# Performance work log

Measured on AMD Instinct MI355X. Metric: run time of the kernel, lower is better.

## Reference

```python
import jax, jax.numpy as jnp
import numpy as np
from jax.ops import segment_sum

N_NODES = 50000
N_EDGES = 50000
N_GRAPHS = 1024


def _inv_deg(idx, num_segments):
    deg = segment_sum(jnp.ones(idx.shape[0], jnp.float32), idx, num_segments=num_segments)
    return jnp.where(deg > 0, 1.0 / deg, 0.0)


def hypergraph_conv(x, W, b, node_idx, edge_idx):
    # PyG HypergraphConv (use_attention=False, heads=1, hyperedge_weight=1):
    # out = D^{-1} H B^{-1} H^T (X W) + b
    D = _inv_deg(node_idx, N_NODES)   # inverse node degree [N]
    B = _inv_deg(edge_idx, N_EDGES)   # inverse hyperedge degree [E]
    xl = x @ W                         # [N, out]
    # node -> hyperedge aggregation
    edge_feat = B[:, None] * segment_sum(xl[node_idx], edge_idx, num_segments=N_EDGES)
    # hyperedge -> node aggregation
    out = D[:, None] * segment_sum(edge_feat[edge_idx], node_idx, num_segments=N_NODES)
    return out + b


def global_mean_pool(x, batch):
    s = segment_sum(x, batch, num_segments=N_GRAPHS)
    cnt = segment_sum(jnp.ones(x.shape[0], jnp.float32), batch, num_segments=N_GRAPHS)
    return s / jnp.maximum(cnt, 1.0)[:, None]


def setup_inputs() -> dict:
    key = jax.random.key(0)
    ks = jax.random.split(key, 16)
    F, H = 128, 256
    def lin(k, fi, fo):
        s = 1.0 / np.sqrt(fi)
        k1, k2 = jax.random.split(k)
        return (jax.random.uniform(k1, (fi, fo), jnp.float32, -s, s),
                jax.random.uniform(k2, (fo,), jnp.float32, -s, s))
    W1, b1 = lin(ks[0], F, H)
    W2, b2 = lin(ks[1], H, 2 * H)
    W3, b3 = lin(ks[2], 2 * H, H)
    Wl1, bl1 = lin(ks[3], H, H // 2)
    Wl2, bl2 = lin(ks[4], H // 2, 1)
    x = jax.random.normal(ks[5], (N_NODES, F), jnp.float32)
    hyperedge_index = jax.random.randint(ks[6], (2, 400000), 0, N_EDGES, jnp.int64)
    batch = jnp.sort(jax.random.randint(ks[7], (N_NODES,), 0, N_GRAPHS, jnp.int64))
    return {"x": x, "hyperedge_index": hyperedge_index, "batch": batch,
            "W1": W1, "b1": b1, "W2": W2, "b2": b2, "W3": W3, "b3": b3,
            "Wl1": Wl1, "bl1": bl1, "Wl2": Wl2, "bl2": bl2}


def reference(x, hyperedge_index, batch, W1, b1, W2, b2, W3, b3, Wl1, bl1, Wl2, bl2):
    node_idx, edge_idx = hyperedge_index[0], hyperedge_index[1]
    h = jax.nn.relu(hypergraph_conv(x, W1, b1, node_idx, edge_idx))
    h = jax.nn.relu(hypergraph_conv(h, W2, b2, node_idx, edge_idx))
    h = jax.nn.relu(hypergraph_conv(h, W3, b3, node_idx, edge_idx))
    g = global_mean_pool(h, batch)              # [G, H]
    g = jax.nn.relu(g @ Wl1 + bl1)
    out = g @ Wl2 + bl2                          # [G, 1]
    return out
```

## Files before the change

### kernel.cpp

```cpp
#include <hip/hip_runtime.h>
#include <hip/hip_bf16.h>

#define N_NODES  50000
#define N_EDGES  50000
#define N_INC    400000
#define N_GRAPHS 1024
#define M_PAD    50048
#define SEG_CAP  50176

typedef __bf16 bf16x8 __attribute__((ext_vector_type(8)));
typedef float  f32x4  __attribute__((ext_vector_type(4)));

__device__ __forceinline__ unsigned short f2bf(float f) {
    __hip_bfloat16 h = __float2bfloat16(f);
    return __builtin_bit_cast(unsigned short, h);
}
__device__ __forceinline__ float bflo(unsigned int u) {
    return __builtin_bit_cast(float, u << 16);
}
__device__ __forceinline__ float bfhi(unsigned int u) {
    return __builtin_bit_cast(float, u & 0xffff0000u);
}
__device__ __forceinline__ unsigned int packbf(float a, float b) {
    return (unsigned int)f2bf(a) | ((unsigned int)f2bf(b) << 16);
}
__device__ __forceinline__ void load_lds16(const unsigned short* g, unsigned short* l) {
    __builtin_amdgcn_global_load_lds((const __attribute__((address_space(1))) void*)g,
                                     (__attribute__((address_space(3))) void*)l, 16, 0, 0);
}

__global__ __launch_bounds__(256) void normhist_kernel(const int* __restrict__ hei,
                                                       const int* __restrict__ braw,
                                                       int* __restrict__ nidx, int* __restrict__ eidx,
                                                       int* __restrict__ bidx,
                                                       int* __restrict__ ndeg, int* __restrict__ edeg,
                                                       int* __restrict__ gcnt) {
    __shared__ int s32;
    int t = threadIdx.x;
    if (t == 0) s32 = 0;
    __syncthreads();
    int probe = hei[4 * t + 1] | hei[4 * t + 3];
    if (probe) s32 = 1;
    __syncthreads();
    int is32 = s32;
    int i = blockIdx.x * 256 + t;
    if (i < N_INC) {
        int n, e;
        if (is32) { n = hei[i];     e = hei[N_INC + i]; }
        else      { n = hei[2 * i]; e = hei[2 * N_INC + 2 * i]; }
        nidx[i] = n; eidx[i] = e;
        atomicAdd(&ndeg[n], 1);
        atomicAdd(&edeg[e], 1);
    }
    if (i < N_NODES) {
        int b = is32 ? braw[i] : braw[2 * i];
        bidx[i] = b;
        atomicAdd(&gcnt[b], 1);
    }
}

__global__ __launch_bounds__(256) void scan_up_f(const int* __restrict__ edeg,
                                                 const int* __restrict__ ndeg,
                                                 const int* __restrict__ gcnt,
                                                 int* __restrict__ eoff, int* __restrict__ noff,
                                                 int* __restrict__ goff,
                                                 int* __restrict__ partials) {
    __shared__ int lds[256];
    int b = blockIdx.x, t = threadIdx.x;
    const int* in; int* outp; int lb;
    if (b < 49)      { in = edeg; outp = eoff; lb = b; }
    else if (b < 98) { in = ndeg; outp = noff; lb = b - 49; }
    else             { in = gcnt; outp = goff; lb = 0; }
    int base = lb * 1024 + t * 4;
    int4 v = *(const int4*)(in + base);
    int s = v.x + v.y + v.z + v.w;
    lds[t] = s;
    __syncthreads();
    for (int off = 1; off < 256; off <<= 1) {
        int u = (t >= off) ? lds[t - off] : 0;
        __syncthreads();
        lds[t] += u;
        __syncthreads();
    }
    int excl = lds[t] - s;
    if (t == 255) partials[b] = lds[255];
    int4 o;
    o.x = excl;
    o.y = excl + v.x;
    o.z = o.y + v.y;
    o.w = o.z + v.z;
    *(int4*)(outp + base) = o;
}

__global__ __launch_bounds__(128) void scan_mid_f(int* __restrict__ partials) {
    __shared__ int lds[99];
    int t = threadIdx.x;
    if (t < 99) lds[t] = partials[t];
    __syncthreads();
    if (t < 3) {
        int lo = (t == 0) ? 0 : (t == 1 ? 49 : 98);
        int hi = (t == 0) ? 49 : (t == 1 ? 98 : 99);
        int run = 0;
        for (int i = lo; i < hi; ++i) { int x = lds[i]; lds[i] = run; run += x; }
    }
    __syncthreads();
    if (t < 99) partials[t] = lds[t];
}

__global__ __launch_bounds__(256) void scan_down_f(int* __restrict__ eoff, int* __restrict__ ecur,
                                                   int* __restrict__ noff, int* __restrict__ ncur,
                                                   int* __restrict__ goff,
                                                   const int* __restrict__ partials) {
    int b = blockIdx.x, t = threadIdx.x;
    int* outp; int* out2; int lb;
    if (b < 49)      { outp = eoff; out2 = ecur; lb = b; }
    else if (b < 98) { outp = noff; out2 = ncur; lb = b - 49; }
    else             { outp = goff; out2 = goff; lb = 0; }
    int base = lb * 1024 + t * 4;
    int p = partials[b];
    int4 v = *(const int4*)(outp + base);
    v.x += p; v.y += p; v.z += p; v.w += p;
    *(int4*)(outp + base) = v;
    *(int4*)(out2 + base) = v;
}

#define NB_CSR  1563
#define NB_CONV 6250
#define NB_W1   128
#define NB_W2   512
#define NB_W3   512
__global__ __launch_bounds__(256) void prep_kernel(const int* __restrict__ nidx,
                                                   const int* __restrict__ eidx,
                                                   int* __restrict__ ecur, int* __restrict__ ncur,
                                                   int* __restrict__ csre, int* __restrict__ csrn,
                                                   const float* __restrict__ x,
                                                   unsigned short* __restrict__ xbf,
                                                   const float* __restrict__ W1, unsigned short* __restrict__ wt1,
                                                   const float* __restrict__ W2, unsigned short* __restrict__ wt2,
                                                   const float* __restrict__ W3, unsigned short* __restrict__ wt3) {
    int b = blockIdx.x, t = threadIdx.x;
    if (b < NB_CSR) {
        int i = b * 256 + t;
        if (i < N_INC) {
            int n = nidx[i], e = eidx[i];
            int p = atomicAdd(&ecur[e], 1);
            csre[p] = n;
            int q = atomicAdd(&ncur[n], 1);
            csrn[q] = e;
        }
    } else if (b < NB_CSR + NB_CONV) {
        int i = (b - NB_CSR) * 256 + t;
        float4 v = *(const float4*)(x + 4 * (size_t)i);
        ushort4 o;
        o.x = f2bf(v.x); o.y = f2bf(v.y); o.z = f2bf(v.z); o.w = f2bf(v.w);
        *(ushort4*)(xbf + 4 * (size_t)i) = o;
    } else if (b < NB_CSR + NB_CONV + NB_W1) {
        int i = (b - NB_CSR - NB_CONV) * 256 + t;
        int k = i >> 8, n = i & 255;
        wt1[n * 128 + k] = f2bf(W1[i]);
    } else if (b < NB_CSR + NB_CONV + NB_W1 + NB_W2) {
        int i = (b - NB_CSR - NB_CONV - NB_W1) * 256 + t;
        int k = i >> 9, n = i & 511;
        wt2[n * 256 + k] = f2bf(W2[i]);
    } else {
        int i = (b - NB_CSR - NB_CONV - NB_W1 - NB_W2) * 256 + t;
        int k = i >> 8, n = i & 255;
        wt3[n * 512 + k] = f2bf(W3[i]);
    }
}

template <bool EPI>
__global__ __launch_bounds__(256) void gemm128_kernel(const unsigned short* __restrict__ A,
                                                      const unsigned short* __restrict__ Bt,
                                                      const float* __restrict__ bias,
                                                      unsigned short* __restrict__ C,
                                                      int M, int K, int N) {
    __shared__ unsigned short As[128 * 32];
    __shared__ unsigned short Bs[128 * 32];
    __shared__ unsigned short Cs[32][140];
    int tid  = threadIdx.x;
    int wave = tid >> 6, lane = tid & 63;
    int n0 = blockIdx.x * 128, m0 = blockIdx.y * 128;
    int quad = lane >> 4, fr = lane & 15;
    int wr = wave >> 1, wc = wave & 1;
    int lrow16 = lane >> 2;
    int lchunk = (lane & 3) * 8;

    const unsigned short* gsrc;
    unsigned short* ldst;
    if (wave < 2) { gsrc = A  + (size_t)(m0 + wave * 64) * K;       ldst = As + wave * 64 * 32; }
    else          { gsrc = Bt + (size_t)(n0 + (wave - 2) * 64) * K; ldst = Bs + (wave - 2) * 64 * 32; }

    f32x4 acc[4][4];
#pragma unroll
    for (int s = 0; s < 4; ++s)
#pragma unroll
        for (int c = 0; c < 4; ++c) acc[s][c] = (f32x4){0.f, 0.f, 0.f, 0.f};

    for (int k0 = 0; k0 < K; k0 += 32) {
#pragma unroll
        for (int l = 0; l < 4; ++l) {
            const unsigned short* g = gsrc + (size_t)(l * 16 + lrow16) * K + k0 + lchunk;
            load_lds16(g, ldst + l * 16 * 32);
        }
        __syncthreads();
        bf16x8 af[4], bfr[4];
#pragma unroll
        for (int s = 0; s < 4; ++s)
            af[s] = *(const bf16x8*)&As[(wr * 64 + s * 16 + fr) * 32 + quad * 8];
#pragma unroll
        for (int c = 0; c < 4; ++c)
            bfr[c] = *(const bf16x8*)&Bs[(wc * 64 + c * 16 + fr) * 32 + quad * 8];
#pragma unroll
        for (int s = 0; s < 4; ++s)
#pragma unroll
            for (int c = 0; c < 4; ++c)
                acc[s][c] = __builtin_amdgcn_mfma_f32_16x16x32_bf16(af[s], bfr[c], acc[s][c], 0, 0, 0);
        __syncthreads();
    }

    float bv[4];
#pragma unroll
    for (int c = 0; c < 4; ++c) bv[c] = EPI ? bias[n0 + wc * 64 + c * 16 + fr] : 0.f;
#pragma unroll
    for (int s = 0; s < 4; ++s) {
#pragma unroll
        for (int c = 0; c < 4; ++c)
#pragma unroll
            for (int r = 0; r < 4; ++r) {
                float v = acc[s][c][r];
                if (EPI) v = fmaxf(v + bv[c], 0.f);
                Cs[wr * 16 + quad * 4 + r][wc * 64 + c * 16 + fr] = f2bf(v);
            }
        __syncthreads();
#pragma unroll
        for (int i = 0; i < 2; ++i) {
            int rl  = i * 16 + (tid >> 4);
            int col = (tid & 15) * 8;
            int gm  = m0 + (rl >> 4) * 64 + s * 16 + (rl & 15);
            if (gm < M) {
                uint4 v = *(const uint4*)&Cs[rl][col];
                *(uint4*)&C[(size_t)gm * N + n0 + col] = v;
            }
        }
        __syncthreads();
    }
}

template <int C, bool BIAS>
__device__ __forceinline__ void seg_body(const unsigned short* __restrict__ in,
                                         const int* __restrict__ offs,
                                         const int* __restrict__ degs,
                                         const int* __restrict__ csr_src,
                                         const float* __restrict__ bias,
                                         unsigned short* __restrict__ outp,
                                         int nseg) {
    constexpr int VEC = C / 64;
    constexpr int NW  = VEC / 2;
    int w = (blockIdx.x * 256 + threadIdx.x) >> 6;
    int lane = threadIdx.x & 63;
    if (w >= nseg) return;
    int deg   = __builtin_amdgcn_readfirstlane(degs[w]);
    int start = __builtin_amdgcn_readfirstlane(offs[w]);
    float dinv = (deg > 0) ? 1.0f / (float)deg : 0.0f;
    const int* cs = csr_src + start;
    float acc[VEC];
#pragma unroll
    for (int q = 0; q < VEC; ++q) acc[q] = 0.f;
    size_t lbase = (size_t)lane * VEC;

    auto accum = [&](unsigned int* v) {
#pragma unroll
        for (int q = 0; q < NW; ++q) { acc[2 * q] += bflo(v[q]); acc[2 * q + 1] += bfhi(v[q]); }
    };
    auto loadrow = [&](int src, unsigned int* v) {
        const unsigned int* p = (const unsigned int*)(in + (size_t)src * C + lbase);
        if constexpr (NW == 4)      { uint4 t = *(const uint4*)p; v[0] = t.x; v[1] = t.y; v[2] = t.z; v[3] = t.w; }
        else if constexpr (NW == 2) { uint2 t = *(const uint2*)p; v[0] = t.x; v[1] = t.y; }
        else                        { v[0] = *p; }
    };

    int j = 0;
    for (; j + 8 <= deg; j += 8) {
        int s[8];
        unsigned int v[8][NW];
#pragma unroll
        for (int u = 0; u < 8; ++u) s[u] = __builtin_amdgcn_readfirstlane(cs[j + u]);
#pragma unroll
        for (int u = 0; u < 8; ++u) loadrow(s[u], v[u]);
#pragma unroll
        for (int u = 0; u < 8; ++u) accum(v[u]);
    }
    for (; j + 4 <= deg; j += 4) {
        int s[4];
        unsigned int v[4][NW];
#pragma unroll
        for (int u = 0; u < 4; ++u) s[u] = __builtin_amdgcn_readfirstlane(cs[j + u]);
#pragma unroll
        for (int u = 0; u < 4; ++u) loadrow(s[u], v[u]);
#pragma unroll
        for (int u = 0; u < 4; ++u) accum(v[u]);
    }
    for (; j < deg; ++j) {
        int s0 = __builtin_amdgcn_readfirstlane(cs[j]);
        unsigned int v0[NW];
        loadrow(s0, v0);
        accum(v0);
    }

    unsigned int o[NW];
#pragma unroll
    for (int q = 0; q < NW; ++q) {
        float a = acc[2 * q] * dinv;
        float b = acc[2 * q + 1] * dinv;
        if constexpr (BIAS) {
            a = fmaxf(a + bias[lbase + 2 * q], 0.f);
            b = fmaxf(b + bias[lbase + 2 * q + 1], 0.f);
        }
        o[q] = packbf(a, b);
    }
    unsigned int* po = (unsigned int*)(outp + (size_t)w * C + lbase);
    if constexpr (NW == 4)      { *(uint4*)po = make_uint4(o[0], o[1], o[2], o[3]); }
    else if constexpr (NW == 2) { *(uint2*)po = make_uint2(o[0], o[1]); }
    else                        { *po = o[0]; }
}

template <int C>
__global__ __launch_bounds__(256) void seg_edge_t(const unsigned short* __restrict__ xl,
                                                  const int* __restrict__ eoff,
                                                  const int* __restrict__ edeg,
                                                  const int* __restrict__ csr_src,
                                                  unsigned short* __restrict__ ef) {
    seg_body<C, false>(xl, eoff, edeg, csr_src, nullptr, ef, N_EDGES);
}

template <int C, bool BIAS>
__global__ __launch_bounds__(256) void seg_node_t(const unsigned short* __restrict__ ef,
                                                  const int* __restrict__ noff,
                                                  const int* __restrict__ ndeg,
                                                  const int* __restrict__ csr_src,
                                                  const float* __restrict__ bias,
                                                  unsigned short* __restrict__ hout) {
    seg_body<C, BIAS>(ef, noff, ndeg, csr_src, bias, hout, N_NODES);
}

__global__ __launch_bounds__(256) void pool_head_kernel(const unsigned short* __restrict__ h,
                                                        const int* __restrict__ goff,
                                                        const int* __restrict__ gcnt,
                                                        const float* __restrict__ Wl1,
                                                        const float* __restrict__ bl1,
                                                        const float* __restrict__ Wl2,
                                                        const float* __restrict__ bl2,
                                                        float* __restrict__ out) {
    __shared__ float xs[256];
    __shared__ float red[128];
    int g = blockIdx.x, t = threadIdx.x;
    int s = goff[g], cnt = gcnt[g];
    float acc = 0.f;
    for (int i = 0; i < cnt; ++i) {
        unsigned int u = h[(size_t)(s + i) * 256 + t];
        acc += __builtin_bit_cast(float, u << 16);
    }
    xs[t] = acc / (float)(cnt > 0 ? cnt : 1);
    __syncthreads();
    if (t < 128) {
        float s2 = 0.f;
        for (int f = 0; f < 256; ++f) s2 += xs[f] * Wl1[f * 128 + t];
        s2 = fmaxf(s2 + bl1[t], 0.f);
        red[t] = s2 * Wl2[t];
    }
    __syncthreads();
    for (int off = 64; off > 0; off >>= 1) {
        if (t < off) red[t] += red[t + off];
        __syncthreads();
    }
    if (t == 0) out[g] = red[0] + bl2[0];
}

extern "C" void kernel_launch(void* const* d_in, const int* in_sizes, int n_in,
                              void* d_out, int out_size, void* d_ws, size_t ws_size,
                              hipStream_t stream) {
    const float* x     = (const float*)d_in[0];
    const int* hei     = (const int*)d_in[1];
    const int* braw    = (const int*)d_in[2];
    const float* W1    = (const float*)d_in[3];
    const float* b1    = (const float*)d_in[4];
    const float* W2    = (const float*)d_in[5];
    const float* b2    = (const float*)d_in[6];
    const float* W3    = (const float*)d_in[7];
    const float* b3    = (const float*)d_in[8];
    const float* Wl1   = (const float*)d_in[9];
    const float* bl1   = (const float*)d_in[10];
    const float* Wl2   = (const float*)d_in[11];
    const float* bl2   = (const float*)d_in[12];
    float* out         = (float*)d_out;

    char* w = (char*)d_ws;
    size_t off = 0;
    auto alloc = [&](size_t bytes) { size_t p = off; off += (bytes + 255) & ~(size_t)255; return p; };
    size_t o_edeg = alloc((size_t)SEG_CAP * 4);
    size_t o_ndeg = alloc((size_t)SEG_CAP * 4);
    size_t o_gcnt = alloc((size_t)1024 * 4);
    size_t zero_end = off;
    size_t o_eoff = alloc((size_t)SEG_CAP * 4);
    size_t o_noff = alloc((size_t)SEG_CAP * 4);
    size_t o_goff = alloc((size_t)1024 * 4);
    size_t o_ecur = alloc((size_t)SEG_CAP * 4);
    size_t o_ncur = alloc((size_t)SEG_CAP * 4);
    size_t o_part = alloc(128 * 4);
    size_t o_nidx = alloc((size_t)N_INC * 4);
    size_t o_eidx = alloc((size_t)N_INC * 4);
    size_t o_bidx = alloc((size_t)N_NODES * 4);
    size_t o_csre = alloc((size_t)N_INC * 4);
    size_t o_csrn = alloc((size_t)N_INC * 4);
    size_t o_wt1  = alloc((size_t)128 * 256 * 2);
    size_t o_wt2  = alloc((size_t)256 * 512 * 2);
    size_t o_wt3  = alloc((size_t)512 * 256 * 2);
    size_t o_xbf  = alloc((size_t)M_PAD * 128 * 2);
    size_t o_Y    = alloc((size_t)M_PAD * 256 * 2);
    size_t o_H1   = alloc((size_t)M_PAD * 256 * 2);
    size_t o_H2   = alloc((size_t)M_PAD * 512 * 2);
    size_t o_bufE = alloc((size_t)N_EDGES * 256 * 2);

    int* edeg = (int*)(w + o_edeg);
    int* ndeg = (int*)(w + o_ndeg);
    int* gcnt = (int*)(w + o_gcnt);
    int* eoff = (int*)(w + o_eoff);
    int* noff = (int*)(w + o_noff);
    int* goff = (int*)(w + o_goff);
    int* ecur = (int*)(w + o_ecur);
    int* ncur = (int*)(w + o_ncur);
    int* part = (int*)(w + o_part);
    int* nidx = (int*)(w + o_nidx);
    int* eidx = (int*)(w + o_eidx);
    int* bidx = (int*)(w + o_bidx);
    int* csre = (int*)(w + o_csre);
    int* csrn = (int*)(w + o_csrn);
    unsigned short* wt1  = (unsigned short*)(w + o_wt1);
    unsigned short* wt2  = (unsigned short*)(w + o_wt2);
    unsigned short* wt3  = (unsigned short*)(w + o_wt3);
    unsigned short* xbf  = (unsigned short*)(w + o_xbf);
    unsigned short* Y    = (unsigned short*)(w + o_Y);
    unsigned short* H1   = (unsigned short*)(w + o_H1);
    unsigned short* H2   = (unsigned short*)(w + o_H2);
    unsigned short* bufE = (unsigned short*)(w + o_bufE);

    hipMemsetAsync(w, 0, zero_end, stream);
    normhist_kernel<<<(N_INC + 255) / 256, 256, 0, stream>>>(hei, braw, nidx, eidx, bidx,
                                                             ndeg, edeg, gcnt);
    scan_up_f<<<99, 256, 0, stream>>>(edeg, ndeg, gcnt, eoff, noff, goff, part);
    scan_mid_f<<<1, 128, 0, stream>>>(part);
    scan_down_f<<<99, 256, 0, stream>>>(eoff, ecur, noff, ncur, goff, part);
    prep_kernel<<<NB_CSR + NB_CONV + NB_W1 + NB_W2 + NB_W3, 256, 0, stream>>>(
        nidx, eidx, ecur, ncur, csre, csrn, x, xbf, W1, wt1, W2, wt2, W3, wt3);

    int segGrid = (N_NODES * 64 + 255) / 256;

    seg_edge_t<128><<<segGrid, 256, 0, stream>>>(xbf, eoff, edeg, csre, bufE);
    seg_node_t<128, false><<<segGrid, 256, 0, stream>>>(bufE, noff, ndeg, csrn, nullptr, Y);
    {
        dim3 grid(256 / 128, M_PAD / 128);
        gemm128_kernel<true><<<grid, 256, 0, stream>>>(Y, wt1, b1, H1, N_NODES, 128, 256);
    }
    seg_edge_t<256><<<segGrid, 256, 0, stream>>>(H1, eoff, edeg, csre, bufE);
    seg_node_t<256, false><<<segGrid, 256, 0, stream>>>(bufE, noff, ndeg, csrn, nullptr, Y);
    {
        dim3 grid(512 / 128, M_PAD / 128);
        gemm128_kernel<true><<<grid, 256, 0, stream>>>(Y, wt2, b2, H2, N_NODES, 256, 512);
    }
    {
        dim3 grid(256 / 128, M_PAD / 128);
        gemm128_kernel<false><<<grid, 256, 0, stream>>>(H2, wt3, nullptr, Y, N_NODES, 512, 256);
    }
    seg_edge_t<256><<<segGrid, 256, 0, stream>>>(Y, eoff, edeg, csre, bufE);
    seg_node_t<256, true><<<segGrid, 256, 0, stream>>>(bufE, noff, ndeg, csrn, b3, H1);

    pool_head_kernel<<<N_GRAPHS, 256, 0, stream>>>(H1, goff, gcnt, Wl1, bl1, Wl2, bl2, out);
}
```

Before: 462.5 us.

## Build CSR from histogram ranks and store indices as 16-bit

Each incidence's rank within its segment is now captured from the histogram atomics. CSR scatter then needs no second round of atomics and no cursor arrays. CSR source indices are stored as unsigned short, halving index traffic in the segment-sum kernels, and compiler memory barriers separate the load and accumulate phases. The 16-bit format assumes node and edge counts stay below 65536 and per-segment degree fits in 16 bits. The unused batch index array is also dropped.

```diff
diff --git a/kernel.cpp b/kernel.cpp
--- a/kernel.cpp
+++ b/kernel.cpp
@@ -32,9 +32,11 @@
 __global__ __launch_bounds__(256) void normhist_kernel(const int* __restrict__ hei,
                                                        const int* __restrict__ braw,
                                                        int* __restrict__ nidx, int* __restrict__ eidx,
-                                                       int* __restrict__ bidx,
+                                                       unsigned short* __restrict__ rn,
+                                                       unsigned short* __restrict__ re,
                                                        int* __restrict__ ndeg, int* __restrict__ edeg,
-                                                       int* __restrict__ gcnt) {
+                                                       int* __restrict__ gcnt,
+                                                       int* __restrict__ goff_src) {
     __shared__ int s32;
     int t = threadIdx.x;
     if (t == 0) s32 = 0;
@@ -49,12 +51,12 @@
         if (is32) { n = hei[i];     e = hei[N_INC + i]; }
         else      { n = hei[2 * i]; e = hei[2 * N_INC + 2 * i]; }
         nidx[i] = n; eidx[i] = e;
-        atomicAdd(&ndeg[n], 1);
-        atomicAdd(&edeg[e], 1);
+        rn[i] = (unsigned short)atomicAdd(&ndeg[n], 1);
+        re[i] = (unsigned short)atomicAdd(&edeg[e], 1);
     }
     if (i < N_NODES) {
         int b = is32 ? braw[i] : braw[2 * i];
-        bidx[i] = b;
+        (void)goff_src;
         atomicAdd(&gcnt[b], 1);
     }
 }
@@ -107,21 +109,20 @@
     if (t < 99) partials[t] = lds[t];
 }
 
-__global__ __launch_bounds__(256) void scan_down_f(int* __restrict__ eoff, int* __restrict__ ecur,
-                                                   int* __restrict__ noff, int* __restrict__ ncur,
+__global__ __launch_bounds__(256) void scan_down_f(int* __restrict__ eoff,
+                                                   int* __restrict__ noff,
                                                    int* __restrict__ goff,
                                                    const int* __restrict__ partials) {
     int b = blockIdx.x, t = threadIdx.x;
-    int* outp; int* out2; int lb;
-    if (b < 49)      { outp = eoff; out2 = ecur; lb = b; }
-    else if (b < 98) { outp = noff; out2 = ncur; lb = b - 49; }
-    else             { outp = goff; out2 = goff; lb = 0; }
+    int* outp; int lb;
+    if (b < 49)      { outp = eoff; lb = b; }
+    else if (b < 98) { outp = noff; lb = b - 49; }
+    else             { outp = goff; lb = 0; }
     int base = lb * 1024 + t * 4;
     int p = partials[b];
     int4 v = *(const int4*)(outp + base);
     v.x += p; v.y += p; v.z += p; v.w += p;
     *(int4*)(outp + base) = v;
-    *(int4*)(out2 + base) = v;
 }
 
 #define NB_CSR  1563
@@ -131,8 +132,12 @@
 #define NB_W3   512
 __global__ __launch_bounds__(256) void prep_kernel(const int* __restrict__ nidx,
                                                    const int* __restrict__ eidx,
-                                                   int* __restrict__ ecur, int* __restrict__ ncur,
-                                                   int* __restrict__ csre, int* __restrict__ csrn,
+                                                   const unsigned short* __restrict__ rn,
+                                                   const unsigned short* __restrict__ re,
+                                                   const int* __restrict__ eoff,
+                                                   const int* __restrict__ noff,
+                                                   unsigned short* __restrict__ csre,
+                                                   unsigned short* __restrict__ csrn,
                                                    const float* __restrict__ x,
                                                    unsigned short* __restrict__ xbf,
                                                    const float* __restrict__ W1, unsigned short* __restrict__ wt1,
@@ -143,10 +148,8 @@
         int i = b * 256 + t;
         if (i < N_INC) {
             int n = nidx[i], e = eidx[i];
-            int p = atomicAdd(&ecur[e], 1);
-            csre[p] = n;
-            int q = atomicAdd(&ncur[n], 1);
-            csrn[q] = e;
+            csre[eoff[e] + re[i]] = (unsigned short)n;
+            csrn[noff[n] + rn[i]] = (unsigned short)e;
         }
     } else if (b < NB_CSR + NB_CONV) {
         int i = (b - NB_CSR) * 256 + t;
@@ -251,7 +254,7 @@
 __device__ __forceinline__ void seg_body(const unsigned short* __restrict__ in,
                                          const int* __restrict__ offs,
                                          const int* __restrict__ degs,
-                                         const int* __restrict__ csr_src,
+                                         const unsigned short* __restrict__ csr_src,
                                          const float* __restrict__ bias,
                                          unsigned short* __restrict__ outp,
                                          int nseg) {
@@ -263,7 +266,7 @@
     int deg   = __builtin_amdgcn_readfirstlane(degs[w]);
     int start = __builtin_amdgcn_readfirstlane(offs[w]);
     float dinv = (deg > 0) ? 1.0f / (float)deg : 0.0f;
-    const int* cs = csr_src + start;
+    const unsigned short* cs = csr_src + start;
     float acc[VEC];
 #pragma unroll
     for (int q = 0; q < VEC; ++q) acc[q] = 0.f;
@@ -285,9 +288,10 @@
         int s[8];
         unsigned int v[8][NW];
 #pragma unroll
-        for (int u = 0; u < 8; ++u) s[u] = __builtin_amdgcn_readfirstlane(cs[j + u]);
+        for (int u = 0; u < 8; ++u) s[u] = __builtin_amdgcn_readfirstlane((int)cs[j + u]);
 #pragma unroll
         for (int u = 0; u < 8; ++u) loadrow(s[u], v[u]);
+        __asm__ __volatile__("" ::: "memory");
 #pragma unroll
         for (int u = 0; u < 8; ++u) accum(v[u]);
     }
@@ -295,14 +299,15 @@
         int s[4];
         unsigned int v[4][NW];
 #pragma unroll
-        for (int u = 0; u < 4; ++u) s[u] = __builtin_amdgcn_readfirstlane(cs[j + u]);
+        for (int u = 0; u < 4; ++u) s[u] = __builtin_amdgcn_readfirstlane((int)cs[j + u]);
 #pragma unroll
         for (int u = 0; u < 4; ++u) loadrow(s[u], v[u]);
+        __asm__ __volatile__("" ::: "memory");
 #pragma unroll
         for (int u = 0; u < 4; ++u) accum(v[u]);
     }
     for (; j < deg; ++j) {
-        int s0 = __builtin_amdgcn_readfirstlane(cs[j]);
+        int s0 = __builtin_amdgcn_readfirstlane((int)cs[j]);
         unsigned int v0[NW];
         loadrow(s0, v0);
         accum(v0);
@@ -329,7 +334,7 @@
 __global__ __launch_bounds__(256) void seg_edge_t(const unsigned short* __restrict__ xl,
                                                   const int* __restrict__ eoff,
                                                   const int* __restrict__ edeg,
-                                                  const int* __restrict__ csr_src,
+                                                  const unsigned short* __restrict__ csr_src,
                                                   unsigned short* __restrict__ ef) {
     seg_body<C, false>(xl, eoff, edeg, csr_src, nullptr, ef, N_EDGES);
 }
@@ -338,7 +343,7 @@
 __global__ __launch_bounds__(256) void seg_node_t(const unsigned short* __restrict__ ef,
                                                   const int* __restrict__ noff,
                                                   const int* __restrict__ ndeg,
-                                                  const int* __restrict__ csr_src,
+                                                  const unsigned short* __restrict__ csr_src,
                                                   const float* __restrict__ bias,
                                                   unsigned short* __restrict__ hout) {
     seg_body<C, BIAS>(ef, noff, ndeg, csr_src, bias, hout, N_NODES);
@@ -405,14 +410,13 @@
     size_t o_eoff = alloc((size_t)SEG_CAP * 4);
     size_t o_noff = alloc((size_t)SEG_CAP * 4);
     size_t o_goff = alloc((size_t)1024 * 4);
-    size_t o_ecur = alloc((size_t)SEG_CAP * 4);
-    size_t o_ncur = alloc((size_t)SEG_CAP * 4);
     size_t o_part = alloc(128 * 4);
     size_t o_nidx = alloc((size_t)N_INC * 4);
     size_t o_eidx = alloc((size_t)N_INC * 4);
-    size_t o_bidx = alloc((size_t)N_NODES * 4);
-    size_t o_csre = alloc((size_t)N_INC * 4);
-    size_t o_csrn = alloc((size_t)N_INC * 4);
+    size_t o_rn   = alloc((size_t)N_INC * 2);
+    size_t o_re   = alloc((size_t)N_INC * 2);
+    size_t o_csre = alloc((size_t)N_INC * 2);
+    size_t o_csrn = alloc((size_t)N_INC * 2);
     size_t o_wt1  = alloc((size_t)128 * 256 * 2);
     size_t o_wt2  = alloc((size_t)256 * 512 * 2);
     size_t o_wt3  = alloc((size_t)512 * 256 * 2);
@@ -428,14 +432,13 @@
     int* eoff = (int*)(w + o_eoff);
     int* noff = (int*)(w + o_noff);
     int* goff = (int*)(w + o_goff);
-    int* ecur = (int*)(w + o_ecur);
-    int* ncur = (int*)(w + o_ncur);
     int* part = (int*)(w + o_part);
     int* nidx = (int*)(w + o_nidx);
     int* eidx = (int*)(w + o_eidx);
-    int* bidx = (int*)(w + o_bidx);
-    int* csre = (int*)(w + o_csre);
-    int* csrn = (int*)(w + o_csrn);
+    unsigned short* rn   = (unsigned short*)(w + o_rn);
+    unsigned short* re   = (unsigned short*)(w + o_re);
+    unsigned short* csre = (unsigned short*)(w + o_csre);
+    unsigned short* csrn = (unsigned short*)(w + o_csrn);
     unsigned short* wt1  = (unsigned short*)(w + o_wt1);
     unsigned short* wt2  = (unsigned short*)(w + o_wt2);
     unsigned short* wt3  = (unsigned short*)(w + o_wt3);
@@ -446,13 +449,13 @@
     unsigned short* bufE = (unsigned short*)(w + o_bufE);
 
     hipMemsetAsync(w, 0, zero_end, stream);
-    normhist_kernel<<<(N_INC + 255) / 256, 256, 0, stream>>>(hei, braw, nidx, eidx, bidx,
-                                                             ndeg, edeg, gcnt);
+    normhist_kernel<<<(N_INC + 255) / 256, 256, 0, stream>>>(hei, braw, nidx, eidx, rn, re,
+                                                             ndeg, edeg, gcnt, goff);
     scan_up_f<<<99, 256, 0, stream>>>(edeg, ndeg, gcnt, eoff, noff, goff, part);
     scan_mid_f<<<1, 128, 0, stream>>>(part);
-    scan_down_f<<<99, 256, 0, stream>>>(eoff, ecur, noff, ncur, goff, part);
+    scan_down_f<<<99, 256, 0, stream>>>(eoff, noff, goff, part);
     prep_kernel<<<NB_CSR + NB_CONV + NB_W1 + NB_W2 + NB_W3, 256, 0, stream>>>(
-        nidx, eidx, ecur, ncur, csre, csrn, x, xbf, W1, wt1, W2, wt2, W3, wt3);
+        nidx, eidx, rn, re, eoff, noff, csre, csrn, x, xbf, W1, wt1, W2, wt2, W3, wt3);
 
     int segGrid = (N_NODES * 64 + 255) / 256;
 
```

Measured after the change: 442.3 us. 1.05x faster.
